# Performance work log

Measured on AMD Instinct MI355X. Metric: run time of the kernel, lower is better.

Reference implementation:

```python
import jax, jax.numpy as jnp
import numpy as np

CLASSES = 80
CELLS = 7
SEG = CLASSES + 5        # per-cell segment: [x, y, w, h, conf, class_scores...]
NCELLS = CELLS ** 2
BATCH = 16384


def setup_inputs() -> dict:
    key = jax.random.key(0)
    x = jax.random.normal(key, (BATCH, NCELLS * SEG), dtype=jnp.float32)
    return {"input_": x}


def reference(input_):
    B = input_.shape[0]
    x = input_.reshape(B, NCELLS, SEG)
    # Original loop only processes the first NCELLS-1 cells (off-by-one kept faithfully).
    act = x[:, : NCELLS - 1, :]                      # [B, 48, SEG]
    box_xy = jax.nn.sigmoid(act[..., 0:2])           # sigmoid on x,y
    wh = act[..., 2:4]                               # untouched
    conf = jax.nn.sigmoid(act[..., 4:5])             # sigmoid on confidence
    cls = jax.nn.softmax(act[..., 5:], axis=-1)      # softmax over class scores
    act_out = jnp.concatenate([box_xy, wh, conf, cls], axis=-1)
    out = jnp.concatenate([act_out, x[:, NCELLS - 1 :, :]], axis=1)
    return out.reshape(B, NCELLS * SEG)
```

## Files before the change

kernel.cpp:

```cpp
#include <hip/hip_runtime.h>
#include <math.h>


#define SEG 85
#define NCELLS 49
#define TPB 64
#define WORDS_PER_BLK (TPB * SEG)
#define F4_PER_BLK (WORDS_PER_BLK / 4)
#define FULL_SWEEPS (F4_PER_BLK / TPB)
#define TAIL (F4_PER_BLK - FULL_SWEEPS * TPB)

#define GLOAD_LDS16(g, l)                                   \
  __builtin_amdgcn_global_load_lds(                         \
      (const __attribute__((address_space(1))) void*)(g),   \
      (__attribute__((address_space(3))) void*)(l), 16, 0, 0)

__global__ __launch_bounds__(TPB) void yolo_act_kernel(
    const float* __restrict__ in, float* __restrict__ out) {
  __shared__ __align__(16) float lds[WORDS_PER_BLK];
  __shared__ float inv_s[TPB + 1];

  const int tid = threadIdx.x;
  const long long blk_word = (long long)blockIdx.x * WORDS_PER_BLK;

  {
    const float* gsrc = in + blk_word;
    #pragma unroll
    for (int it = 0; it < FULL_SWEEPS; ++it)
      GLOAD_LDS16(gsrc + (it * TPB + tid) * 4, lds + it * TPB * 4);
    if (tid < TAIL)
      GLOAD_LDS16(gsrc + (FULL_SWEEPS * TPB + tid) * 4,
                  lds + FULL_SWEEPS * TPB * 4);
  }
  __syncthreads();

  {
    const int seg_global = blockIdx.x * TPB + tid;
    const int cell = seg_global % NCELLS;
    float* p = lds + tid * SEG;
    if (cell != NCELLS - 1) {
      float s0 = 0.f, s1 = 0.f, s2 = 0.f, s3 = 0.f;
      #pragma unroll
      for (int i = 5; i < SEG; i += 4) {
        float e0 = __expf(p[i + 0]);
        float e1 = __expf(p[i + 1]);
        float e2 = __expf(p[i + 2]);
        float e3 = __expf(p[i + 3]);
        p[i + 0] = e0; p[i + 1] = e1; p[i + 2] = e2; p[i + 3] = e3;
        s0 += e0; s1 += e1; s2 += e2; s3 += e3;
      }
      p[0] = 1.f / (1.f + __expf(-p[0]));
      p[1] = 1.f / (1.f + __expf(-p[1]));
      p[4] = 1.f / (1.f + __expf(-p[4]));
      inv_s[tid] = 1.f / ((s0 + s1) + (s2 + s3));
    } else {
      inv_s[tid] = -1.f;
    }
    if (tid == 0) inv_s[TPB] = -1.f;
  }
  __syncthreads();

  {
    float4* __restrict__ gdst = (float4*)(out + blk_word);
    const float4* lsrc = (const float4*)lds;
    #pragma unroll
    for (int it = 0; it <= FULL_SWEEPS; ++it) {
      const int k = tid + it * TPB;
      if (it == FULL_SWEEPS && tid >= TAIL) break;
      float4 v = lsrc[k];
      const int w = k * 4;
      const int seg0 = w / SEG;
      const int off0 = w - seg0 * SEG;
      const float sc0 = inv_s[seg0];
      const float sc1 = inv_s[seg0 + 1];
      float r[4] = {v.x, v.y, v.z, v.w};
      #pragma unroll
      for (int j = 0; j < 4; ++j) {
        const int o = off0 + j;
        const bool cross = (o >= SEG);
        const float sc = cross ? sc1 : sc0;
        const int off = cross ? (o - SEG) : o;
        if (off >= 5 && sc > 0.f) r[j] *= sc;
      }
      v.x = r[0]; v.y = r[1]; v.z = r[2]; v.w = r[3];
      gdst[k] = v;
    }
  }
}

extern "C" void kernel_launch(void* const* d_in, const int* in_sizes, int n_in,
                              void* d_out, int out_size, void* d_ws, size_t ws_size,
                              hipStream_t stream) {
  const float* in = (const float*)d_in[0];
  float* out = (float*)d_out;
  const int nseg = in_sizes[0] / SEG;
  const int grid = nseg / TPB;
  yolo_act_kernel<<<grid, TPB, 0, stream>>>(in, out);
}
```

Before: 440.1 us.

## Make activation kernel persistent with double-buffered LDS prefetch

Turns the one-tile-per-block kernel into a persistent grid of up to 768 single-wave blocks that stride over tiles. The next tile is prefetched into a second LDS buffer with global_load_lds while the current tile's softmax, sigmoid and stores run. Manual s_waitcnt vmcnt thresholds replace the __syncthreads barriers and rely on in-order vector memory counter retirement, stores included. The aim is to hide load latency and cut per-block launch overhead. The cost is lower occupancy, from fewer waves per CU and doubled LDS per block, plus fragile hand-tuned wait counts.

After: 449.1 us. +2.1%, slower.

```diff
diff --git a/kernel.cpp b/kernel.cpp
--- a/kernel.cpp
+++ b/kernel.cpp
@@ -5,10 +5,11 @@
 #define SEG 85
 #define NCELLS 49
 #define TPB 64
-#define WORDS_PER_BLK (TPB * SEG)
-#define F4_PER_BLK (WORDS_PER_BLK / 4)
-#define FULL_SWEEPS (F4_PER_BLK / TPB)
-#define TAIL (F4_PER_BLK - FULL_SWEEPS * TPB)
+#define WORDS_PER_TILE (TPB * SEG)
+#define F4_PER_TILE (WORDS_PER_TILE / 4)
+#define FULL_SWEEPS (F4_PER_TILE / TPB)
+#define TAIL (F4_PER_TILE - FULL_SWEEPS * TPB)
+#define PERSIST_BLOCKS 768
 
 #define GLOAD_LDS16(g, l)                                   \
   __builtin_amdgcn_global_load_lds(                         \
@@ -16,75 +17,109 @@
       (__attribute__((address_space(3))) void*)(l), 16, 0, 0)
 
 __global__ __launch_bounds__(TPB) void yolo_act_kernel(
-    const float* __restrict__ in, float* __restrict__ out) {
-  __shared__ __align__(16) float lds[WORDS_PER_BLK];
-  __shared__ float inv_s[TPB + 1];
+    const float* __restrict__ in, float* __restrict__ out, int ntiles) {
+  __shared__ __align__(16) float lds[2][WORDS_PER_TILE];
+  __shared__ float inv_s[2][TPB + 1];
 
   const int tid = threadIdx.x;
-  const long long blk_word = (long long)blockIdx.x * WORDS_PER_BLK;
+
+  int t = blockIdx.x;
+  if (t >= ntiles) return;
 
   {
-    const float* gsrc = in + blk_word;
+    const float* gsrc = in + (long long)t * WORDS_PER_TILE;
     #pragma unroll
     for (int it = 0; it < FULL_SWEEPS; ++it)
-      GLOAD_LDS16(gsrc + (it * TPB + tid) * 4, lds + it * TPB * 4);
+      GLOAD_LDS16(gsrc + (it * TPB + tid) * 4, &lds[0][it * TPB * 4]);
     if (tid < TAIL)
       GLOAD_LDS16(gsrc + (FULL_SWEEPS * TPB + tid) * 4,
-                  lds + FULL_SWEEPS * TPB * 4);
+                  &lds[0][FULL_SWEEPS * TPB * 4]);
   }
-  __syncthreads();
 
-  {
-    const int seg_global = blockIdx.x * TPB + tid;
-    const int cell = seg_global % NCELLS;
-    float* p = lds + tid * SEG;
-    if (cell != NCELLS - 1) {
-      float s0 = 0.f, s1 = 0.f, s2 = 0.f, s3 = 0.f;
+  int buf = 0;
+  bool has_prev = false;
+
+  while (true) {
+    const int tnext = t + gridDim.x;
+    const bool has_next = (tnext < ntiles);
+
+    if (has_next) {
+      const float* gsrc = in + (long long)tnext * WORDS_PER_TILE;
+      float* l = &lds[buf ^ 1][0];
       #pragma unroll
-      for (int i = 5; i < SEG; i += 4) {
-        float e0 = __expf(p[i + 0]);
-        float e1 = __expf(p[i + 1]);
-        float e2 = __expf(p[i + 2]);
-        float e3 = __expf(p[i + 3]);
-        p[i + 0] = e0; p[i + 1] = e1; p[i + 2] = e2; p[i + 3] = e3;
-        s0 += e0; s1 += e1; s2 += e2; s3 += e3;
+      for (int it = 0; it < FULL_SWEEPS; ++it)
+        GLOAD_LDS16(gsrc + (it * TPB + tid) * 4, l + it * TPB * 4);
+      if (tid < TAIL)
+        GLOAD_LDS16(gsrc + (FULL_SWEEPS * TPB + tid) * 4,
+                    l + FULL_SWEEPS * TPB * 4);
+    }
+
+    if (has_prev && has_next)
+      asm volatile("s_waitcnt vmcnt(44)" ::: "memory");
+    else if (has_prev || has_next)
+      asm volatile("s_waitcnt vmcnt(22)" ::: "memory");
+    else
+      asm volatile("s_waitcnt vmcnt(0)" ::: "memory");
+    __builtin_amdgcn_sched_barrier(0);
+
+    {
+      const int seg_global = t * TPB + tid;
+      const int cell = seg_global % NCELLS;
+      float* p = &lds[buf][tid * SEG];
+      if (cell != NCELLS - 1) {
+        float s0 = 0.f, s1 = 0.f, s2 = 0.f, s3 = 0.f;
+        #pragma unroll
+        for (int i = 5; i < SEG; i += 4) {
+          float e0 = __expf(p[i + 0]);
+          float e1 = __expf(p[i + 1]);
+          float e2 = __expf(p[i + 2]);
+          float e3 = __expf(p[i + 3]);
+          p[i + 0] = e0; p[i + 1] = e1; p[i + 2] = e2; p[i + 3] = e3;
+          s0 += e0; s1 += e1; s2 += e2; s3 += e3;
+        }
+        p[0] = 1.f / (1.f + __expf(-p[0]));
+        p[1] = 1.f / (1.f + __expf(-p[1]));
+        p[4] = 1.f / (1.f + __expf(-p[4]));
+        inv_s[buf][tid] = 1.f / ((s0 + s1) + (s2 + s3));
+      } else {
+        inv_s[buf][tid] = -1.f;
       }
-      p[0] = 1.f / (1.f + __expf(-p[0]));
-      p[1] = 1.f / (1.f + __expf(-p[1]));
-      p[4] = 1.f / (1.f + __expf(-p[4]));
-      inv_s[tid] = 1.f / ((s0 + s1) + (s2 + s3));
-    } else {
-      inv_s[tid] = -1.f;
+      if (tid == 0) inv_s[buf][TPB] = -1.f;
     }
-    if (tid == 0) inv_s[TPB] = -1.f;
-  }
-  __syncthreads();
 
-  {
-    float4* __restrict__ gdst = (float4*)(out + blk_word);
-    const float4* lsrc = (const float4*)lds;
-    #pragma unroll
-    for (int it = 0; it <= FULL_SWEEPS; ++it) {
-      const int k = tid + it * TPB;
-      if (it == FULL_SWEEPS && tid >= TAIL) break;
-      float4 v = lsrc[k];
-      const int w = k * 4;
-      const int seg0 = w / SEG;
-      const int off0 = w - seg0 * SEG;
-      const float sc0 = inv_s[seg0];
-      const float sc1 = inv_s[seg0 + 1];
-      float r[4] = {v.x, v.y, v.z, v.w};
+    {
+      float4* __restrict__ gdst =
+          (float4*)(out + (long long)t * WORDS_PER_TILE);
+      const float4* lsrc = (const float4*)&lds[buf][0];
+      const float* inv = &inv_s[buf][0];
       #pragma unroll
-      for (int j = 0; j < 4; ++j) {
-        const int o = off0 + j;
-        const bool cross = (o >= SEG);
-        const float sc = cross ? sc1 : sc0;
-        const int off = cross ? (o - SEG) : o;
-        if (off >= 5 && sc > 0.f) r[j] *= sc;
+      for (int it = 0; it <= FULL_SWEEPS; ++it) {
+        if (it == FULL_SWEEPS && tid >= TAIL) break;
+        const int k = tid + it * TPB;
+        float4 v = lsrc[k];
+        const int w = k * 4;
+        const int seg0 = w / SEG;
+        const int off0 = w - seg0 * SEG;
+        const float sc0 = inv[seg0];
+        const float sc1 = inv[seg0 + 1];
+        float r[4] = {v.x, v.y, v.z, v.w};
+        #pragma unroll
+        for (int j = 0; j < 4; ++j) {
+          const int o = off0 + j;
+          const bool cross = (o >= SEG);
+          const float sc = cross ? sc1 : sc0;
+          const int off = cross ? (o - SEG) : o;
+          if (off >= 5 && sc > 0.f) r[j] *= sc;
+        }
+        v.x = r[0]; v.y = r[1]; v.z = r[2]; v.w = r[3];
+        gdst[k] = v;
       }
-      v.x = r[0]; v.y = r[1]; v.z = r[2]; v.w = r[3];
-      gdst[k] = v;
     }
+
+    if (!has_next) break;
+    t = tnext;
+    buf ^= 1;
+    has_prev = true;
   }
 }
 
@@ -94,6 +129,7 @@
   const float* in = (const float*)d_in[0];
   float* out = (float*)d_out;
   const int nseg = in_sizes[0] / SEG;
-  const int grid = nseg / TPB;
-  yolo_act_kernel<<<grid, TPB, 0, stream>>>(in, out);
+  const int ntiles = nseg / TPB;
+  const int grid = (ntiles < PERSIST_BLOCKS) ? ntiles : PERSIST_BLOCKS;
+  yolo_act_kernel<<<grid, TPB, 0, stream>>>(in, out, ntiles);
 }
```
